# Kernel optimization log

Hardware: AMD Instinct MI355X
Metric: run time of the kernel (lower is better)

## Reference

```python
import jax, jax.numpy as jnp
import numpy as np

NX, NY, NZ = 432, 496, 1   # grid_size (nx, ny, nz), nz must be 1
NBEV = 128                 # NUM_BEV_FEATURES
K = 4                      # NUM_K
SHRINK = 0.0025            # SHRINK_TH
BN_EPS = 1e-3


def setup_inputs():
    key = jax.random.key(0)
    ks = jax.random.split(key, 8)
    B, P, NPT, D, M = 2, 6000, 4096, 64, 1024
    pillar_features = jax.random.normal(ks[0], (B, P, D), jnp.float32)
    point_features = jax.random.normal(ks[1], (B, NPT, D), jnp.float32)
    # unique flat BEV cells per scene -> coords columns (z, y, x) as in OpenPCDet coords[:,1:4]
    coords = []
    for b in range(B):
        flat = jax.random.permutation(jax.random.fold_in(ks[2], b), NX * NY)[:P]
        y = flat // NX
        x = flat % NX
        z = jnp.zeros_like(flat)
        coords.append(jnp.stack([z, y, x], axis=1))
    voxel_coords = jnp.stack(coords, 0).astype(jnp.int32)
    adapt_w = jax.random.normal(ks[3], (NBEV // 2, D * K), jnp.float32) * 0.05  # Linear(no bias)
    mem_w = jax.random.normal(ks[4], (M, D), jnp.float32) * 0.05               # MemoryUnit slots
    bn_gamma = jnp.ones((NBEV // 2,), jnp.float32)
    bn_beta = jnp.zeros((NBEV // 2,), jnp.float32)
    return dict(pillar_features=pillar_features, point_features=point_features,
                voxel_coords=voxel_coords, adapt_w=adapt_w, mem_w=mem_w,
                bn_gamma=bn_gamma, bn_beta=bn_beta)


def _forward(pillar_features, point_features, voxel_coords, adapt_w, mem_w, bn_gamma, bn_beta):
    def per_batch(pillars, points, coords):
        # pillars [P,D], points [Np,D], coords [P,3] = (z, y, x)
        # get_score: softmax over points dim, top-k points per pillar
        score = jax.nn.softmax(pillars @ points.T, axis=1)            # [P,Np]
        _, idx = jax.lax.top_k(score, K)                              # [P,K] (indices detached)
        pts = points[idx]                                             # [P,K,D]
        # MemoryUnit (MemAE-style): softmax attention over memory, hard-shrink-relu, L1 renorm
        x = pts.reshape(-1, points.shape[1])                          # [P*K,D]
        att = jax.nn.softmax(x @ mem_w.T, axis=1)                     # [P*K,M]
        shr = jax.nn.relu(att - SHRINK) * att / (jnp.abs(att - SHRINK) + 1e-12)
        att = shr / (jnp.sum(jnp.abs(shr), axis=1, keepdims=True) + 1e-12)
        mem_out = (att @ mem_w).reshape(pillars.shape[0], -1)         # [P, K*D]
        # adapt_layer (Linear, no bias) -> BatchNorm1d (training stats over pillars) -> ReLU
        h = mem_out @ adapt_w.T                                       # [P, NBEV//2]
        mu = jnp.mean(h, axis=0)
        var = jnp.var(h, axis=0)
        h = (h - mu) / jnp.sqrt(var + BN_EPS) * bn_gamma + bn_beta
        h = jax.nn.relu(h)
        feats = jnp.concatenate([pillars, h], axis=1)                 # [P, NBEV]
        # scatter into dense BEV grid: index = z + y*nx + x (nz==1 so z==0)
        flat = coords[:, 0] + coords[:, 1] * NX + coords[:, 2]
        spatial = jnp.zeros((NBEV, NZ * NX * NY), feats.dtype).at[:, flat].set(feats.T)
        pind = jnp.zeros((3, NZ * NX * NY), feats.dtype)
        pind = pind.at[0, flat].set(coords[:, 1].astype(feats.dtype))
        pind = pind.at[1, flat].set(coords[:, 2].astype(feats.dtype))
        pind = pind.at[2, flat].set(coords[:, 0].astype(feats.dtype))
        return spatial, pind

    spatial, pind = jax.vmap(per_batch)(pillar_features, point_features, voxel_coords)
    B = spatial.shape[0]
    return spatial.reshape(B, NBEV * NZ, NY, NX), pind.reshape(B, 3 * NZ, NY, NX)


def reference(pillar_features, point_features, voxel_coords, adapt_w, mem_w, bn_gamma, bn_beta):
    return _forward(pillar_features, point_features, voxel_coords, adapt_w, mem_w, bn_gamma, bn_beta)
```

## Files before the change

### kernel.cpp

```cpp
#include <hip/hip_runtime.h>

#define NXg 432
#define NYg 496
#define SCELLS (NXg*NYg)
#define PB 6000
#define NPTS 4096
#define DD 64
#define MM 1024
#define KK 4
#define BB 2
#define NROWS (PB*KK)
#define NSEG 16
#define SEGPTS (NPTS/NSEG)
#define CHROWS 64
#define NCHNK (SEGPTS/CHROWS)
#define SHRINK_TH 0.0025f
#define BN_EPS 1e-3f
#define NEG_INF -3.402823466e38f

#define INS4(v, id, v0,v1,v2,v3, i0,i1,i2,i3) { \
    bool g0 = (v) > v0, g1 = (v) > v1, g2 = (v) > v2; \
    v3 = g2 ? v2 : (v);              i3 = g2 ? i2 : (id); \
    v2 = g2 ? (g1 ? v1 : (v)) : v2;  i2 = g2 ? (g1 ? i1 : (id)) : i2; \
    v1 = g1 ? (g0 ? v0 : (v)) : v1;  i1 = g1 ? (g0 ? i0 : (id)) : i1; \
    v0 = g0 ? (v) : v0;              i0 = g0 ? (id) : i0; \
}

__global__ __launch_bounds__(256) void k_init_inv(int* __restrict__ inv) {
    int i = blockIdx.x*256 + threadIdx.x;
    inv[i] = -1;
}

__global__ __launch_bounds__(256) void k_scatter_inv(const int* __restrict__ coords,
                                                     int* __restrict__ inv) {
    int i = blockIdx.x*256 + threadIdx.x;
    if (i >= BB*PB) return;
    int b = i / PB, p = i % PB;
    const int* c = coords + (size_t)i*3;
    int flat = c[0] + c[1]*NXg + c[2];
    inv[b*SCELLS + flat] = p;
}

__global__ __launch_bounds__(256) void k_score_topk(const float* __restrict__ pillars,
                                                    const float* __restrict__ points,
                                                    float* __restrict__ pV,
                                                    int* __restrict__ pI) {
    __shared__ float4 sPt[CHROWS*16];
    const int b = blockIdx.y;
    const int seg = blockIdx.z;
    const int t = threadIdx.x;
    const int pillar = blockIdx.x*256 + t;
    const int prow = pillar < PB ? pillar : PB-1;
    const int j0 = seg * SEGPTS;

    const float4* pil4  = (const float4*)pillars;
    const float4* ptsB4 = (const float4*)(points + (size_t)b*NPTS*DD);

    float4 wreg[16];
    #pragma unroll
    for (int d4 = 0; d4 < 16; d4++)
        wreg[d4] = pil4[((size_t)b*PB + prow)*16 + d4];

    float tv0=NEG_INF, tv1=NEG_INF, tv2=NEG_INF, tv3=NEG_INF;
    int   ti0=0, ti1=0, ti2=0, ti3=0;

    for (int ch = 0; ch < NCHNK; ch++) {
        const float4* src = ptsB4 + (size_t)(j0 + ch*CHROWS)*16;
        for (int i = t; i < CHROWS*16; i += 256)
            sPt[i] = src[i];
        __syncthreads();

        const int jb = j0 + ch*CHROWS;
        for (int j = 0; j < CHROWS; j += 2) {
            float a0 = 0.f, a1 = 0.f;
            #pragma unroll
            for (int d4 = 0; d4 < 16; d4++) {
                float4 x0 = sPt[j*16 + d4];
                float4 x1 = sPt[(j+1)*16 + d4];
                a0 += wreg[d4].x*x0.x + wreg[d4].y*x0.y + wreg[d4].z*x0.z + wreg[d4].w*x0.w;
                a1 += wreg[d4].x*x1.x + wreg[d4].y*x1.y + wreg[d4].z*x1.z + wreg[d4].w*x1.w;
            }
            if (a0 > tv3) INS4(a0, jb+j,   tv0,tv1,tv2,tv3, ti0,ti1,ti2,ti3)
            if (a1 > tv3) INS4(a1, jb+j+1, tv0,tv1,tv2,tv3, ti0,ti1,ti2,ti3)
        }
        __syncthreads();
    }

    if (pillar < PB) {
        size_t ob = (((size_t)b*NSEG + seg)*PB + pillar)*KK;
        pV[ob+0]=tv0; pV[ob+1]=tv1; pV[ob+2]=tv2; pV[ob+3]=tv3;
        pI[ob+0]=ti0; pI[ob+1]=ti1; pI[ob+2]=ti2; pI[ob+3]=ti3;
    }
}

__global__ __launch_bounds__(256) void k_merge(const float* __restrict__ pV,
                                               const int* __restrict__ pI,
                                               int* __restrict__ idxOut) {
    int i = blockIdx.x*256 + threadIdx.x;
    if (i >= BB*PB) return;
    int b = i / PB, p = i % PB;
    float fv0=NEG_INF, fv1=NEG_INF, fv2=NEG_INF, fv3=NEG_INF;
    int fi0=0, fi1=0, fi2=0, fi3=0;
    for (int s = 0; s < NSEG; s++) {
        size_t base = (((size_t)b*NSEG + s)*PB + p)*KK;
        #pragma unroll
        for (int q = 0; q < 4; q++) {
            float v = pV[base+q];
            if (v > fv3) INS4(v, pI[base+q], fv0,fv1,fv2,fv3, fi0,fi1,fi2,fi3)
        }
    }
    idxOut[(size_t)i*KK+0]=fi0; idxOut[(size_t)i*KK+1]=fi1;
    idxOut[(size_t)i*KK+2]=fi2; idxOut[(size_t)i*KK+3]=fi3;
}

__global__ __launch_bounds__(256) void k_logits(const float* __restrict__ points,
                                                const int* __restrict__ idxIn,
                                                const float* __restrict__ memw,
                                                float* __restrict__ logits,
                                                int b) {
    __shared__ float4 sX4[64*16];
    __shared__ int sId[64];
    const int t = threadIdx.x;
    const int lane = t & 63, wv = t >> 6;
    const int row0 = blockIdx.x * 64;
    const int cg = blockIdx.y * 256 + wv * 64;

    if (t < 64) sId[t] = idxIn[(size_t)b*NROWS + row0 + t];

    const float4* mw4 = (const float4*)memw;
    float4 wreg[16];
    #pragma unroll
    for (int d4 = 0; d4 < 16; d4++) wreg[d4] = mw4[(size_t)(cg + lane)*16 + d4];

    __syncthreads();
    const float4* ptsB4 = (const float4*)(points + (size_t)b*NPTS*DD);
    for (int i = t; i < 1024; i += 256) {
        int r = i >> 4, c = i & 15;
        sX4[i] = ptsB4[(size_t)sId[r]*16 + c];
    }
    __syncthreads();

    for (int r = 0; r < 64; r += 2) {
        float a0 = 0.f, a1 = 0.f;
        #pragma unroll
        for (int d4 = 0; d4 < 16; d4++) {
            float4 x0 = sX4[r*16 + d4];
            float4 x1 = sX4[(r+1)*16 + d4];
            a0 += wreg[d4].x*x0.x + wreg[d4].y*x0.y + wreg[d4].z*x0.z + wreg[d4].w*x0.w;
            a1 += wreg[d4].x*x1.x + wreg[d4].y*x1.y + wreg[d4].z*x1.z + wreg[d4].w*x1.w;
        }
        logits[(size_t)(row0 + r)*MM + cg + lane] = a0;
        logits[(size_t)(row0 + r + 1)*MM + cg + lane] = a1;
    }
}

__global__ __launch_bounds__(256) void k_moG(const float* __restrict__ logits,
                                             const float* __restrict__ memw,
                                             float* __restrict__ mo,
                                             int b) {
    __shared__ __align__(16) char smem[28672];
    float4* sAtt4 = (float4*)smem;
    float4* sW4   = (float4*)(smem + 12288);
    float*  sWf   = (float*)sW4;
    __shared__ float sM[48], sRinv[48], sRsc[48];
    const int t = threadIdx.x;
    const int lane = t & 63, wv = t >> 6;
    const int p0 = blockIdx.x * 12;
    const int row0 = p0 * 4;

    const float4* lg4 = (const float4*)logits;
    #pragma unroll
    for (int rr = 0; rr < 12; rr++) {
        int r = wv*12 + rr;
        size_t base = (size_t)(row0 + r)*256;
        float4 l0 = lg4[base + lane];
        float4 l1 = lg4[base + 64 + lane];
        float4 l2 = lg4[base + 128 + lane];
        float4 l3 = lg4[base + 192 + lane];
        float m = fmaxf(fmaxf(fmaxf(l0.x,l0.y),fmaxf(l0.z,l0.w)),
                 fmaxf(fmaxf(fmaxf(l1.x,l1.y),fmaxf(l1.z,l1.w)),
                 fmaxf(fmaxf(fmaxf(l2.x,l2.y),fmaxf(l2.z,l2.w)),
                       fmaxf(fmaxf(l3.x,l3.y),fmaxf(l3.z,l3.w)))));
        #pragma unroll
        for (int off = 1; off < 64; off <<= 1) m = fmaxf(m, __shfl_xor(m, off));
        l0.x=__expf(l0.x-m); l0.y=__expf(l0.y-m); l0.z=__expf(l0.z-m); l0.w=__expf(l0.w-m);
        l1.x=__expf(l1.x-m); l1.y=__expf(l1.y-m); l1.z=__expf(l1.z-m); l1.w=__expf(l1.w-m);
        l2.x=__expf(l2.x-m); l2.y=__expf(l2.y-m); l2.z=__expf(l2.z-m); l2.w=__expf(l2.w-m);
        l3.x=__expf(l3.x-m); l3.y=__expf(l3.y-m); l3.z=__expf(l3.z-m); l3.w=__expf(l3.w-m);
        float s = (l0.x+l0.y+l0.z+l0.w) + (l1.x+l1.y+l1.z+l1.w)
                + (l2.x+l2.y+l2.z+l2.w) + (l3.x+l3.y+l3.z+l3.w);
        #pragma unroll
        for (int off = 1; off < 64; off <<= 1) s += __shfl_xor(s, off);
        float rinv = 1.f / s;
        float sh = 0.f;
        {
            float e, tt;
            e=l0.x*rinv; tt=e-SHRINK_TH; sh += tt>0.f ? e*tt/(tt+1e-12f) : 0.f;
            e=l0.y*rinv; tt=e-SHRINK_TH; sh += tt>0.f ? e*tt/(tt+1e-12f) : 0.f;
            e=l0.z*rinv; tt=e-SHRINK_TH; sh += tt>0.f ? e*tt/(tt+1e-12f) : 0.f;
            e=l0.w*rinv; tt=e-SHRINK_TH; sh += tt>0.f ? e*tt/(tt+1e-12f) : 0.f;
            e=l1.x*rinv; tt=e-SHRINK_TH; sh += tt>0.f ? e*tt/(tt+1e-12f) : 0.f;
            e=l1.y*rinv; tt=e-SHRINK_TH; sh += tt>0.f ? e*tt/(tt+1e-12f) : 0.f;
            e=l1.z*rinv; tt=e-SHRINK_TH; sh += tt>0.f ? e*tt/(tt+1e-12f) : 0.f;
            e=l1.w*rinv; tt=e-SHRINK_TH; sh += tt>0.f ? e*tt/(tt+1e-12f) : 0.f;
            e=l2.x*rinv; tt=e-SHRINK_TH; sh += tt>0.f ? e*tt/(tt+1e-12f) : 0.f;
            e=l2.y*rinv; tt=e-SHRINK_TH; sh += tt>0.f ? e*tt/(tt+1e-12f) : 0.f;
            e=l2.z*rinv; tt=e-SHRINK_TH; sh += tt>0.f ? e*tt/(tt+1e-12f) : 0.f;
            e=l2.w*rinv; tt=e-SHRINK_TH; sh += tt>0.f ? e*tt/(tt+1e-12f) : 0.f;
            e=l3.x*rinv; tt=e-SHRINK_TH; sh += tt>0.f ? e*tt/(tt+1e-12f) : 0.f;
            e=l3.y*rinv; tt=e-SHRINK_TH; sh += tt>0.f ? e*tt/(tt+1e-12f) : 0.f;
            e=l3.z*rinv; tt=e-SHRINK_TH; sh += tt>0.f ? e*tt/(tt+1e-12f) : 0.f;
            e=l3.w*rinv; tt=e-SHRINK_TH; sh += tt>0.f ? e*tt/(tt+1e-12f) : 0.f;
        }
        #pragma unroll
        for (int off = 1; off < 64; off <<= 1) sh += __shfl_xor(sh, off);
        if (lane == 0) { sM[r] = m; sRinv[r] = rinv; sRsc[r] = 1.f/(sh + 1e-12f); }
    }
    __syncthreads();

    float acc[12];
    #pragma unroll
    for (int s=0;s<12;s++) acc[s]=0.f;
    const float4* mw4 = (const float4*)memw;

    for (int tile = 0; tile < 16; tile++) {
        __syncthreads();
        for (int i = t; i < 768; i += 256) {
            int rr = i >> 4, m4 = i & 15;
            float4 lg = lg4[(size_t)(row0 + rr)*256 + tile*16 + m4];
            float m = sM[rr], rinv = sRinv[rr], rsc = sRsc[rr];
            float4 o;
            float e, tt;
            e=__expf(lg.x-m)*rinv; tt=e-SHRINK_TH; o.x = (tt>0.f ? e*tt/(tt+1e-12f) : 0.f)*rsc;
            e=__expf(lg.y-m)*rinv; tt=e-SHRINK_TH; o.y = (tt>0.f ? e*tt/(tt+1e-12f) : 0.f)*rsc;
            e=__expf(lg.z-m)*rinv; tt=e-SHRINK_TH; o.z = (tt>0.f ? e*tt/(tt+1e-12f) : 0.f)*rsc;
            e=__expf(lg.w-m)*rinv; tt=e-SHRINK_TH; o.w = (tt>0.f ? e*tt/(tt+1e-12f) : 0.f)*rsc;
            sAtt4[rr*16 + m4] = o;
        }
        #pragma unroll 4
        for (int i = t; i < 1024; i += 256) {
            int m = i >> 4, c4 = i & 15;
            sW4[m*16 + c4] = mw4[(size_t)(tile*64 + m)*16 + c4];
        }
        __syncthreads();
        #pragma unroll 4
        for (int m4 = 0; m4 < 16; m4++) {
            float w0 = sWf[(m4*4+0)*64 + lane];
            float w1 = sWf[(m4*4+1)*64 + lane];
            float w2 = sWf[(m4*4+2)*64 + lane];
            float w3 = sWf[(m4*4+3)*64 + lane];
            #pragma unroll
            for (int s = 0; s < 12; s++) {
                float4 a4 = sAtt4[(wv + 4*s)*16 + m4];
                acc[s] += a4.x*w0 + a4.y*w1 + a4.z*w2 + a4.w*w3;
            }
        }
    }
    #pragma unroll
    for (int s = 0; s < 12; s++) {
        int r = wv + 4*s;
        mo[(size_t)(p0 + (r >> 2))*256 + (r & 3)*64 + lane] = acc[s];
    }
}

__global__ __launch_bounds__(256) void k_adapt(const float* __restrict__ mo,
                                               const float* __restrict__ adaptw,
                                               float* __restrict__ hOut,
                                               int b) {
    __shared__ __align__(16) char smem[77824];
    float* sMo = (float*)smem;
    float4* sA4 = (float4*)(smem + 12288);
    const int t = threadIdx.x;
    const int lane = t & 63, wv = t >> 6;
    const int p0 = blockIdx.x * 12;

    const float4* mo4 = (const float4*)(mo + (size_t)p0*256);
    float4* sMo4w = (float4*)sMo;
    #pragma unroll
    for (int q = 0; q < 3; q++)
        sMo4w[q*256 + t] = mo4[q*256 + t];
    const float4* adG4 = (const float4*)adaptw;
    for (int i = t; i < 4096; i += 256) {
        int c = i >> 6, j4 = i & 63;
        sA4[c*64 + (j4 ^ (c & 15))] = adG4[c*64 + j4];
    }
    __syncthreads();
    const float4* sMo4 = (const float4*)sMo;
    float h0=0.f, h1=0.f, h2=0.f;
    #pragma unroll 8
    for (int j4 = 0; j4 < 64; j4++) {
        float4 a4 = sA4[lane*64 + (j4 ^ (lane & 15))];
        int sub = (j4 >> 4)*16 + (j4 & 15);
        float4 q0 = sMo4[(4*(wv+0))*16 + sub];
        float4 q1 = sMo4[(4*(wv+4))*16 + sub];
        float4 q2 = sMo4[(4*(wv+8))*16 + sub];
        h0 += q0.x*a4.x + q0.y*a4.y + q0.z*a4.z + q0.w*a4.w;
        h1 += q1.x*a4.x + q1.y*a4.y + q1.z*a4.z + q1.w*a4.w;
        h2 += q2.x*a4.x + q2.y*a4.y + q2.z*a4.z + q2.w*a4.w;
    }
    hOut[((size_t)b*PB + p0 + wv + 0)*DD + lane] = h0;
    hOut[((size_t)b*PB + p0 + wv + 4)*DD + lane] = h1;
    hOut[((size_t)b*PB + p0 + wv + 8)*DD + lane] = h2;
}

__global__ __launch_bounds__(256) void k_bn1(const float* __restrict__ h,
                                             float* __restrict__ pSum,
                                             float* __restrict__ pSq) {
    const int bid = blockIdx.x;
    const int b = bid >> 5, ch = bid & 31;
    const int r0 = ch*188;
    int r1 = r0 + 188; if (r1 > PB) r1 = PB;
    __shared__ float sS[4*64], sS2[4*64];
    const int t = threadIdx.x;
    const int c = t & 63, stripe = t >> 6;
    float s = 0.f, s2 = 0.f;
    for (int r = r0 + stripe; r < r1; r += 4) {
        float v = h[((size_t)b*PB + r)*DD + c];
        s += v; s2 += v*v;
    }
    sS[stripe*64 + c] = s; sS2[stripe*64 + c] = s2;
    __syncthreads();
    if (t < 64) {
        float ts = sS[t] + sS[64+t] + sS[128+t] + sS[192+t];
        float ts2 = sS2[t] + sS2[64+t] + sS2[128+t] + sS2[192+t];
        pSum[(size_t)bid*64 + t] = ts;
        pSq[(size_t)bid*64 + t] = ts2;
    }
}

__global__ __launch_bounds__(64) void k_bn2(const float* __restrict__ pSum,
                                            const float* __restrict__ pSq,
                                            const float* __restrict__ gamma,
                                            float* __restrict__ bnMu,
                                            float* __restrict__ bnScale) {
    const int b = blockIdx.x;
    const int t = threadIdx.x;
    float ts = 0.f, ts2 = 0.f;
    for (int ch = 0; ch < 32; ch++) {
        ts += pSum[(size_t)(b*32 + ch)*64 + t];
        ts2 += pSq[(size_t)(b*32 + ch)*64 + t];
    }
    float mu = ts / (float)PB;
    float var = ts2 / (float)PB - mu*mu;
    if (var < 0.f) var = 0.f;
    bnMu[b*64+t] = mu;
    bnScale[b*64+t] = gamma[t] / sqrtf(var + BN_EPS);
}

__global__ __launch_bounds__(256) void k_fill(const int* __restrict__ inv,
                                              const float* __restrict__ pillars,
                                              const float* __restrict__ h,
                                              const float* __restrict__ bnMu,
                                              const float* __restrict__ bnScale,
                                              const float* __restrict__ beta,
                                              float* __restrict__ out) {
    const int b = blockIdx.y;
    const int f = blockIdx.x*256 + threadIdx.x;
    __shared__ float sMu[64], sSc[64], sBe[64];
    if (threadIdx.x < 64) {
        sMu[threadIdx.x] = bnMu[b*64+threadIdx.x];
        sSc[threadIdx.x] = bnScale[b*64+threadIdx.x];
        sBe[threadIdx.x] = beta[threadIdx.x];
    }
    __syncthreads();
    int iv = inv[b*SCELLS + f];
    bool occ = iv >= 0;
    int iv0 = occ ? iv : 0;
    float* sp = out + (size_t)b*128*SCELLS;
    const float* prow = pillars + ((size_t)b*PB + iv0)*DD;
    const float* hrow = h + ((size_t)b*PB + iv0)*DD;
    #pragma unroll 4
    for (int c = 0; c < 64; c++)
        sp[(size_t)c*SCELLS + f] = occ ? prow[c] : 0.f;
    #pragma unroll 4
    for (int c = 0; c < 64; c++) {
        float v = 0.f;
        if (occ) {
            float hv = hrow[c];
            v = fmaxf((hv - sMu[c])*sSc[c] + sBe[c], 0.f);
        }
        sp[(size_t)(64+c)*SCELLS + f] = v;
    }
    float* pi = out + (size_t)BB*128*SCELLS + (size_t)b*3*SCELLS;
    pi[f]              = occ ? (float)(f / NXg) : 0.f;
    pi[SCELLS + f]     = occ ? (float)(f % NXg) : 0.f;
    pi[2*(size_t)SCELLS + f] = 0.f;
}

extern "C" void kernel_launch(void* const* d_in, const int* in_sizes, int n_in,
                              void* d_out, int out_size, void* d_ws, size_t ws_size,
                              hipStream_t stream) {
    const float* pillars = (const float*)d_in[0];
    const float* points  = (const float*)d_in[1];
    const int*   coords  = (const int*)d_in[2];
    const float* adaptw  = (const float*)d_in[3];
    const float* memw    = (const float*)d_in[4];
    const float* gamma   = (const float*)d_in[5];
    const float* beta    = (const float*)d_in[6];
    float* out = (float*)d_out;

    char* w = (char*)d_ws;
    int* inv = (int*)w;        w += (size_t)BB*SCELLS*4;
    int* idx = (int*)w;        w += (size_t)BB*PB*KK*4;
    float* h = (float*)w;      w += (size_t)BB*PB*DD*4;
    float* bnMu = (float*)w;   w += (size_t)BB*64*4;
    float* bnScale = (float*)w; w += (size_t)BB*64*4;
    float* pSum = (float*)w;   w += (size_t)BB*32*64*4;
    float* pSq = (float*)w;    w += (size_t)BB*32*64*4;
    float* mo = (float*)w;     w += (size_t)PB*256*4;
    float* logits = (float*)w;
    float* pV = logits;
    int*   pI = (int*)(logits + (size_t)BB*NSEG*PB*KK);

    k_init_inv<<<dim3(BB*SCELLS/256), dim3(256), 0, stream>>>(inv);
    k_scatter_inv<<<dim3((BB*PB+255)/256), dim3(256), 0, stream>>>(coords, inv);
    k_score_topk<<<dim3((PB+255)/256, BB, NSEG), dim3(256), 0, stream>>>(pillars, points, pV, pI);
    k_merge<<<dim3((BB*PB+255)/256), dim3(256), 0, stream>>>(pV, pI, idx);
    for (int b = 0; b < BB; b++) {
        k_logits<<<dim3(NROWS/64, 4), dim3(256), 0, stream>>>(points, idx, memw, logits, b);
        k_moG<<<dim3(PB/12), dim3(256), 0, stream>>>(logits, memw, mo, b);
        k_adapt<<<dim3(PB/12), dim3(256), 0, stream>>>(mo, adaptw, h, b);
    }
    k_bn1<<<dim3(BB*32), dim3(256), 0, stream>>>(h, pSum, pSq);
    k_bn2<<<dim3(BB), dim3(64), 0, stream>>>(pSum, pSq, gamma, bnMu, bnScale);
    k_fill<<<dim3(SCELLS/256, BB), dim3(256), 0, stream>>>(inv, pillars, h, bnMu, bnScale, beta, out);
}
```

Measured before the change: 765.3 us.

## Register-block two pillars per thread in top-k and halve k_moG pillar tile

The score/top-k kernel now has each thread handle two pillars, so every shared-memory point vector it loads is reused for two dot products. This halves LDS traffic per FLOP and halves the number of blocks. Separately, k_moG now processes 6 pillars per block instead of 12, using less shared memory and more blocks to raise occupancy. The cost is more memory-weight tile reloads per pillar. The top-k change doubles register pressure, which may lower occupancy, and gives fewer blocks (12 x 2 x 16).

```diff
diff --git a/kernel.cpp b/kernel.cpp
--- a/kernel.cpp
+++ b/kernel.cpp
@@ -14,6 +14,7 @@
 #define SEGPTS (NPTS/NSEG)
 #define CHROWS 64
 #define NCHNK (SEGPTS/CHROWS)
+#define MOP 6
 #define SHRINK_TH 0.0025f
 #define BN_EPS 1e-3f
 #define NEG_INF -3.402823466e38f
@@ -49,20 +50,26 @@
     const int b = blockIdx.y;
     const int seg = blockIdx.z;
     const int t = threadIdx.x;
-    const int pillar = blockIdx.x*256 + t;
-    const int prow = pillar < PB ? pillar : PB-1;
+    const int pA = blockIdx.x*512 + t;
+    const int pB = pA + 256;
+    const int prB = pB < PB ? pB : PB-1;
     const int j0 = seg * SEGPTS;
 
     const float4* pil4  = (const float4*)pillars;
     const float4* ptsB4 = (const float4*)(points + (size_t)b*NPTS*DD);
 
-    float4 wreg[16];
+    float4 wA[16], wB[16];
     #pragma unroll
     for (int d4 = 0; d4 < 16; d4++)
-        wreg[d4] = pil4[((size_t)b*PB + prow)*16 + d4];
-
-    float tv0=NEG_INF, tv1=NEG_INF, tv2=NEG_INF, tv3=NEG_INF;
-    int   ti0=0, ti1=0, ti2=0, ti3=0;
+        wA[d4] = pil4[((size_t)b*PB + pA)*16 + d4];
+    #pragma unroll
+    for (int d4 = 0; d4 < 16; d4++)
+        wB[d4] = pil4[((size_t)b*PB + prB)*16 + d4];
+
+    float tvA0=NEG_INF, tvA1=NEG_INF, tvA2=NEG_INF, tvA3=NEG_INF;
+    int   tiA0=0, tiA1=0, tiA2=0, tiA3=0;
+    float tvB0=NEG_INF, tvB1=NEG_INF, tvB2=NEG_INF, tvB3=NEG_INF;
+    int   tiB0=0, tiB1=0, tiB2=0, tiB3=0;
 
     for (int ch = 0; ch < NCHNK; ch++) {
         const float4* src = ptsB4 + (size_t)(j0 + ch*CHROWS)*16;
@@ -72,24 +79,33 @@
 
         const int jb = j0 + ch*CHROWS;
         for (int j = 0; j < CHROWS; j += 2) {
-            float a0 = 0.f, a1 = 0.f;
+            float a0 = 0.f, a1 = 0.f, b0 = 0.f, b1 = 0.f;
             #pragma unroll
             for (int d4 = 0; d4 < 16; d4++) {
                 float4 x0 = sPt[j*16 + d4];
                 float4 x1 = sPt[(j+1)*16 + d4];
-                a0 += wreg[d4].x*x0.x + wreg[d4].y*x0.y + wreg[d4].z*x0.z + wreg[d4].w*x0.w;
-                a1 += wreg[d4].x*x1.x + wreg[d4].y*x1.y + wreg[d4].z*x1.z + wreg[d4].w*x1.w;
+                a0 += wA[d4].x*x0.x + wA[d4].y*x0.y + wA[d4].z*x0.z + wA[d4].w*x0.w;
+                a1 += wA[d4].x*x1.x + wA[d4].y*x1.y + wA[d4].z*x1.z + wA[d4].w*x1.w;
+                b0 += wB[d4].x*x0.x + wB[d4].y*x0.y + wB[d4].z*x0.z + wB[d4].w*x0.w;
+                b1 += wB[d4].x*x1.x + wB[d4].y*x1.y + wB[d4].z*x1.z + wB[d4].w*x1.w;
             }
-            if (a0 > tv3) INS4(a0, jb+j,   tv0,tv1,tv2,tv3, ti0,ti1,ti2,ti3)
-            if (a1 > tv3) INS4(a1, jb+j+1, tv0,tv1,tv2,tv3, ti0,ti1,ti2,ti3)
+            if (a0 > tvA3) INS4(a0, jb+j,   tvA0,tvA1,tvA2,tvA3, tiA0,tiA1,tiA2,tiA3)
+            if (a1 > tvA3) INS4(a1, jb+j+1, tvA0,tvA1,tvA2,tvA3, tiA0,tiA1,tiA2,tiA3)
+            if (b0 > tvB3) INS4(b0, jb+j,   tvB0,tvB1,tvB2,tvB3, tiB0,tiB1,tiB2,tiB3)
+            if (b1 > tvB3) INS4(b1, jb+j+1, tvB0,tvB1,tvB2,tvB3, tiB0,tiB1,tiB2,tiB3)
         }
         __syncthreads();
     }
 
-    if (pillar < PB) {
-        size_t ob = (((size_t)b*NSEG + seg)*PB + pillar)*KK;
-        pV[ob+0]=tv0; pV[ob+1]=tv1; pV[ob+2]=tv2; pV[ob+3]=tv3;
-        pI[ob+0]=ti0; pI[ob+1]=ti1; pI[ob+2]=ti2; pI[ob+3]=ti3;
+    {
+        size_t ob = (((size_t)b*NSEG + seg)*PB + pA)*KK;
+        pV[ob+0]=tvA0; pV[ob+1]=tvA1; pV[ob+2]=tvA2; pV[ob+3]=tvA3;
+        pI[ob+0]=tiA0; pI[ob+1]=tiA1; pI[ob+2]=tiA2; pI[ob+3]=tiA3;
+    }
+    if (pB < PB) {
+        size_t ob = (((size_t)b*NSEG + seg)*PB + pB)*KK;
+        pV[ob+0]=tvB0; pV[ob+1]=tvB1; pV[ob+2]=tvB2; pV[ob+3]=tvB3;
+        pI[ob+0]=tiB0; pI[ob+1]=tiB1; pI[ob+2]=tiB2; pI[ob+3]=tiB3;
     }
 }
 
@@ -158,20 +174,20 @@
                                              const float* __restrict__ memw,
                                              float* __restrict__ mo,
                                              int b) {
-    __shared__ __align__(16) char smem[28672];
+    __shared__ __align__(16) char smem[22528];
     float4* sAtt4 = (float4*)smem;
-    float4* sW4   = (float4*)(smem + 12288);
+    float4* sW4   = (float4*)(smem + 6144);
     float*  sWf   = (float*)sW4;
-    __shared__ float sM[48], sRinv[48], sRsc[48];
+    __shared__ float sM[24], sRinv[24], sRsc[24];
     const int t = threadIdx.x;
     const int lane = t & 63, wv = t >> 6;
-    const int p0 = blockIdx.x * 12;
+    const int p0 = blockIdx.x * MOP;
     const int row0 = p0 * 4;
 
     const float4* lg4 = (const float4*)logits;
     #pragma unroll
-    for (int rr = 0; rr < 12; rr++) {
-        int r = wv*12 + rr;
+    for (int rr = 0; rr < MOP; rr++) {
+        int r = wv*MOP + rr;
         size_t base = (size_t)(row0 + r)*256;
         float4 l0 = lg4[base + lane];
         float4 l1 = lg4[base + 64 + lane];
@@ -218,14 +234,14 @@
     }
     __syncthreads();
 
-    float acc[12];
-    #pragma unroll
-    for (int s=0;s<12;s++) acc[s]=0.f;
+    float acc[MOP];
+    #pragma unroll
+    for (int s=0;s<MOP;s++) acc[s]=0.f;
     const float4* mw4 = (const float4*)memw;
 
     for (int tile = 0; tile < 16; tile++) {
         __syncthreads();
-        for (int i = t; i < 768; i += 256) {
+        for (int i = t; i < 24*16; i += 256) {
             int rr = i >> 4, m4 = i & 15;
             float4 lg = lg4[(size_t)(row0 + rr)*256 + tile*16 + m4];
             float m = sM[rr], rinv = sRinv[rr], rsc = sRsc[rr];
@@ -250,14 +266,14 @@
             float w2 = sWf[(m4*4+2)*64 + lane];
             float w3 = sWf[(m4*4+3)*64 + lane];
             #pragma unroll
-            for (int s = 0; s < 12; s++) {
+            for (int s = 0; s < MOP; s++) {
                 float4 a4 = sAtt4[(wv + 4*s)*16 + m4];
                 acc[s] += a4.x*w0 + a4.y*w1 + a4.z*w2 + a4.w*w3;
             }
         }
     }
     #pragma unroll
-    for (int s = 0; s < 12; s++) {
+    for (int s = 0; s < MOP; s++) {
         int r = wv + 4*s;
         mo[(size_t)(p0 + (r >> 2))*256 + (r & 3)*64 + lane] = acc[s];
     }
@@ -414,11 +430,11 @@
 
     k_init_inv<<<dim3(BB*SCELLS/256), dim3(256), 0, stream>>>(inv);
     k_scatter_inv<<<dim3((BB*PB+255)/256), dim3(256), 0, stream>>>(coords, inv);
-    k_score_topk<<<dim3((PB+255)/256, BB, NSEG), dim3(256), 0, stream>>>(pillars, points, pV, pI);
+    k_score_topk<<<dim3((PB+511)/512, BB, NSEG), dim3(256), 0, stream>>>(pillars, points, pV, pI);
     k_merge<<<dim3((BB*PB+255)/256), dim3(256), 0, stream>>>(pV, pI, idx);
     for (int b = 0; b < BB; b++) {
         k_logits<<<dim3(NROWS/64, 4), dim3(256), 0, stream>>>(points, idx, memw, logits, b);
-        k_moG<<<dim3(PB/12), dim3(256), 0, stream>>>(logits, memw, mo, b);
+        k_moG<<<dim3(PB/MOP), dim3(256), 0, stream>>>(logits, memw, mo, b);
         k_adapt<<<dim3(PB/12), dim3(256), 0, stream>>>(mo, adaptw, h, b);
     }
     k_bn1<<<dim3(BB*32), dim3(256), 0, stream>>>(h, pSum, pSq);
```

New measurement: 912.8 us. 19.3% more time.
